# Optimization experiments

Measured on AMD Instinct MI355X. Metric: run time of the kernel, lower is better.

The kernel has to match this reference:

```python
import jax, jax.numpy as jnp
import numpy as np

N_NODES = 50000
N_EDGES = 800000
IN_DIM_N = 128
IN_DIM_E = 32
OUT_DIM = 128


def setup_inputs() -> dict:
    key = jax.random.key(0)
    k = jax.random.split(key, 6)
    nfeats = jax.random.normal(k[0], (N_NODES, IN_DIM_N), dtype=jnp.float32)
    efeats = jax.random.normal(k[1], (N_EDGES, IN_DIM_E), dtype=jnp.float32)
    # xavier-normal-ish scaling
    W_fc = jax.random.normal(k[2], (OUT_DIM, IN_DIM_N), dtype=jnp.float32) * (2.0 / np.sqrt(IN_DIM_N + OUT_DIM))
    W_attn = jax.random.normal(k[3], (1, 2 * OUT_DIM + IN_DIM_E), dtype=jnp.float32) * 0.08
    src = jax.random.randint(k[4], (N_EDGES,), 0, N_NODES, dtype=jnp.int32)
    dst = jax.random.randint(k[5], (N_EDGES,), 0, N_NODES, dtype=jnp.int32)
    return {"nfeats": nfeats, "efeats": efeats, "W_fc": W_fc, "W_attn": W_attn, "src": src, "dst": dst}


def reference(nfeats, efeats, W_fc, W_attn, src, dst):
    n_nodes = nfeats.shape[0]
    out_dim = W_fc.shape[0]
    in_dim_e = efeats.shape[1]

    # z = fc(nfeats)  [N, out_dim]
    z = nfeats @ W_fc.T

    # attn_fc(cat([z_src, efeats, z_dst])) split into three small dots
    a = W_attn[0]
    a_src = a[:out_dim]
    a_e = a[out_dim:out_dim + in_dim_e]
    a_dst = a[out_dim + in_dim_e:]
    s_src = z @ a_src            # [N]
    s_dst = z @ a_dst            # [N]
    s_e = efeats @ a_e           # [E]

    # per-edge attention logit + leaky_relu (torch default slope 0.01)
    e = jax.nn.leaky_relu(s_src[src] + s_e + s_dst[dst], negative_slope=0.01)  # [E]

    # segment softmax over incoming edges of each dst node
    m = jax.ops.segment_max(e, dst, num_segments=n_nodes)
    m = jnp.where(jnp.isfinite(m), m, 0.0)  # guard zero-degree nodes
    w = jnp.exp(e - m[dst])
    denom = jax.ops.segment_sum(w, dst, num_segments=n_nodes)
    alpha = w / jnp.where(denom > 0, denom, 1.0)[dst]  # [E]

    # weighted sum of source z into dst nodes
    h = jax.ops.segment_sum(alpha[:, None] * z[src], dst, num_segments=n_nodes)  # [N, out_dim]
    return h
```

## Files before the change

kernel.cpp:

```cpp
#include <hip/hip_runtime.h>
#include <math.h>

#define N_NODES 50000
#define N_EDGES 800000
#define IN_DIM_N 128
#define IN_DIM_E 32
#define OUT_DIM 128
#define SCAN_BLOCKS ((N_NODES + 255) / 256)
#define GEMM_BLOCKS ((N_NODES + 63) / 64)

typedef __bf16 bf16x8 __attribute__((ext_vector_type(8)));
typedef float  f32x4  __attribute__((ext_vector_type(4)));

__device__ inline unsigned bf16_rne(float x) {
    unsigned u = __float_as_uint(x);
    return (u + 0x7FFFu + ((u >> 16) & 1u)) >> 16;
}
__device__ inline unsigned pack_bf2(float a, float b) {
    return bf16_rne(a) | (bf16_rne(b) << 16);
}

__launch_bounds__(256)
__global__ void gemm_mfma_kernel(const float* __restrict__ A, const float* __restrict__ W,
                                 const float* __restrict__ attn,
                                 const int* __restrict__ dst, int* __restrict__ counts,
                                 unsigned* __restrict__ zb,
                                 float* __restrict__ s_src, float* __restrict__ s_dst) {
    __shared__ unsigned Au[64 * 68];
    __shared__ unsigned Bu[8192];
    __shared__ float asrc[128], adst[128];
    int tid = threadIdx.x;
    int row0 = blockIdx.x * 64;

    for (int i = tid; i < 2048; i += 256) {
        int fl = i & 63, tile = (i >> 6) & 7, ks = i >> 9;
        int n  = tile * 16 + (fl & 15);
        int kb = ks * 32 + (fl >> 4) * 8;
        const float* srcp = W + n * 128 + kb;
        unsigned o[4];
#pragma unroll
        for (int j = 0; j < 4; ++j) o[j] = pack_bf2(srcp[2 * j], srcp[2 * j + 1]);
        ((uint4*)Bu)[i] = *(uint4*)o;
    }
    if (tid < 128) { asrc[tid] = attn[tid]; adst[tid] = attn[160 + tid]; }

    for (int i = tid; i < 64 * 32; i += 256) {
        int r = i >> 5, q = i & 31;
        int gr = row0 + r;
        float4 v = make_float4(0.f, 0.f, 0.f, 0.f);
        if (gr < N_NODES) v = ((const float4*)A)[(long)gr * 32 + q];
        uint2 p = make_uint2(pack_bf2(v.x, v.y), pack_bf2(v.z, v.w));
        *((uint2*)&Au[r * 68 + q * 2]) = p;
    }
    __syncthreads();

    int lane = tid & 63;
    int wave = tid >> 6;
    int m = lane & 15, quad = lane >> 4;

    f32x4 acc[8];
#pragma unroll
    for (int t = 0; t < 8; ++t) acc[t] = (f32x4){0.f, 0.f, 0.f, 0.f};

#pragma unroll
    for (int ks = 0; ks < 4; ++ks) {
        uint4 au = *((const uint4*)&Au[(wave * 16 + m) * 68 + ks * 16 + quad * 4]);
        bf16x8 af = *(bf16x8*)&au;
#pragma unroll
        for (int t = 0; t < 8; ++t) {
            uint4 bu = *((const uint4*)&Bu[((ks * 8 + t) * 64 + lane) * 4]);
            bf16x8 bf = *(bf16x8*)&bu;
            acc[t] = __builtin_amdgcn_mfma_f32_16x16x32_bf16(af, bf, acc[t], 0, 0, 0);
        }
    }

    float ps[4] = {0.f, 0.f, 0.f, 0.f}, pd[4] = {0.f, 0.f, 0.f, 0.f};
#pragma unroll
    for (int t = 0; t < 8; ++t) {
        float as_ = asrc[t * 16 + m], ad_ = adst[t * 16 + m];
#pragma unroll
        for (int r = 0; r < 4; ++r) {
            float v = acc[t][r];
            ps[r] = fmaf(v, as_, ps[r]);
            pd[r] = fmaf(v, ad_, pd[r]);
            float vn = __shfl_xor(v, 1, 64);
            if (!(m & 1)) {
                int grow = row0 + wave * 16 + quad * 4 + r;
                if (grow < N_NODES)
                    zb[(long)grow * 64 + t * 8 + (m >> 1)] = pack_bf2(v, vn);
            }
        }
    }
#pragma unroll
    for (int r = 0; r < 4; ++r) {
        for (int off = 1; off < 16; off <<= 1) {
            ps[r] += __shfl_xor(ps[r], off, 64);
            pd[r] += __shfl_xor(pd[r], off, 64);
        }
    }
    if (m == 0) {
#pragma unroll
        for (int r = 0; r < 4; ++r) {
            int grow = row0 + wave * 16 + quad * 4 + r;
            if (grow < N_NODES) { s_src[grow] = ps[r]; s_dst[grow] = pd[r]; }
        }
    }

    for (int e = blockIdx.x * 256 + tid; e < N_EDGES; e += GEMM_BLOCKS * 256)
        atomicAdd(&counts[dst[e]], 1);
}

__launch_bounds__(256)
__global__ void scan1_kernel(const int* __restrict__ counts, int* __restrict__ offsets,
                             int* __restrict__ blocksums) {
    int i = blockIdx.x * 256 + threadIdx.x;
    int v = (i < N_NODES) ? counts[i] : 0;
    int lane = threadIdx.x & 63;
    int wv = threadIdx.x >> 6;
    int x = v;
    for (int off = 1; off < 64; off <<= 1) {
        int y = __shfl_up(x, off, 64);
        if (lane >= off) x += y;
    }
    __shared__ int wsum[4];
    if (lane == 63) wsum[wv] = x;
    __syncthreads();
    int base = 0;
    for (int w = 0; w < wv; ++w) base += wsum[w];
    if (i < N_NODES) offsets[i] = base + x - v;
    if (threadIdx.x == 255) blocksums[blockIdx.x] = base + x;
}

__launch_bounds__(256)
__global__ void scan2_kernel(int* __restrict__ blocksums) {
    int t = threadIdx.x;
    int v = (t < SCAN_BLOCKS) ? blocksums[t] : 0;
    int lane = t & 63;
    int wv = t >> 6;
    int x = v;
    for (int off = 1; off < 64; off <<= 1) {
        int y = __shfl_up(x, off, 64);
        if (lane >= off) x += y;
    }
    __shared__ int wsum[4];
    if (lane == 63) wsum[wv] = x;
    __syncthreads();
    int base = 0;
    for (int w = 0; w < wv; ++w) base += wsum[w];
    if (t < SCAN_BLOCKS) blocksums[t] = base + x - v;
}

__launch_bounds__(256)
__global__ void scan3_kernel(int* __restrict__ offsets, const int* __restrict__ blocksums,
                             int* __restrict__ cursor) {
    int i = blockIdx.x * 256 + threadIdx.x;
    if (i < N_NODES) {
        int v = offsets[i] + blocksums[blockIdx.x];
        offsets[i] = v;
        cursor[i] = v;
    }
    if (i == 0) offsets[N_NODES] = N_EDGES;
}

__global__ void score_scatter_kernel(const float* __restrict__ efeats, const float* __restrict__ attn,
                                     const int* __restrict__ src, const int* __restrict__ dst,
                                     const float* __restrict__ s_src, const float* __restrict__ s_dst,
                                     int* __restrict__ cursor, unsigned* __restrict__ pairs4) {
    int i = blockIdx.x * blockDim.x + threadIdx.x;
    if (i >= N_EDGES) return;
    const float4* ef = (const float4*)(efeats + (long)i * IN_DIM_E);
    const float4* ae = (const float4*)(attn + OUT_DIM);
    float se = 0.f;
#pragma unroll
    for (int q = 0; q < IN_DIM_E / 4; ++q) {
        float4 v = ef[q];
        float4 a = ae[q];
        se += v.x * a.x + v.y * a.y + v.z * a.z + v.w * a.w;
    }
    int s = src[i], d = dst[i];
    float x = s_src[s] + se + s_dst[d];
    float ev = (x >= 0.f) ? x : 0.01f * x;
    float w = expf(ev);
    int pos = atomicAdd(&cursor[d], 1);
    pairs4[pos] = (unsigned)s | (bf16_rne(w) << 16);
}

__launch_bounds__(256)
__global__ void aggregate_kernel(const unsigned* __restrict__ pairs4, const int* __restrict__ offsets,
                                 const unsigned* __restrict__ zb, float* __restrict__ h) {
    int node = blockIdx.x * 4 + (threadIdx.x >> 6);
    if (node >= N_NODES) return;
    int lane = threadIdx.x & 63;
    int beg = offsets[node], end = offsets[node + 1];
    float ax0 = 0.f, ay0 = 0.f, ax1 = 0.f, ay1 = 0.f;
    float ax2 = 0.f, ay2 = 0.f, ax3 = 0.f, ay3 = 0.f;
    float dsum = 0.f;
    for (int base = beg; base < end; base += 64) {
        int n = min(64, end - base);
        unsigned u = 0;
        if (lane < n) {
            u = pairs4[base + lane];
            dsum += __uint_as_float(u & 0xFFFF0000u);
        }
        int j = 0;
        for (; j + 3 < n; j += 4) {
            unsigned u0 = (unsigned)__shfl((int)u, j, 64);
            unsigned u1 = (unsigned)__shfl((int)u, j + 1, 64);
            unsigned u2 = (unsigned)__shfl((int)u, j + 2, 64);
            unsigned u3 = (unsigned)__shfl((int)u, j + 3, 64);
            unsigned z0 = zb[(long)(u0 & 0xFFFFu) * 64 + lane];
            unsigned z1 = zb[(long)(u1 & 0xFFFFu) * 64 + lane];
            unsigned z2 = zb[(long)(u2 & 0xFFFFu) * 64 + lane];
            unsigned z3 = zb[(long)(u3 & 0xFFFFu) * 64 + lane];
            float w0 = __uint_as_float(u0 & 0xFFFF0000u);
            float w1 = __uint_as_float(u1 & 0xFFFF0000u);
            float w2 = __uint_as_float(u2 & 0xFFFF0000u);
            float w3 = __uint_as_float(u3 & 0xFFFF0000u);
            ax0 = fmaf(w0, __uint_as_float(z0 << 16), ax0);
            ay0 = fmaf(w0, __uint_as_float(z0 & 0xFFFF0000u), ay0);
            ax1 = fmaf(w1, __uint_as_float(z1 << 16), ax1);
            ay1 = fmaf(w1, __uint_as_float(z1 & 0xFFFF0000u), ay1);
            ax2 = fmaf(w2, __uint_as_float(z2 << 16), ax2);
            ay2 = fmaf(w2, __uint_as_float(z2 & 0xFFFF0000u), ay2);
            ax3 = fmaf(w3, __uint_as_float(z3 << 16), ax3);
            ay3 = fmaf(w3, __uint_as_float(z3 & 0xFFFF0000u), ay3);
        }
        for (; j < n; ++j) {
            unsigned u0 = (unsigned)__shfl((int)u, j, 64);
            unsigned z0 = zb[(long)(u0 & 0xFFFFu) * 64 + lane];
            float w0 = __uint_as_float(u0 & 0xFFFF0000u);
            ax0 = fmaf(w0, __uint_as_float(z0 << 16), ax0);
            ay0 = fmaf(w0, __uint_as_float(z0 & 0xFFFF0000u), ay0);
        }
    }
    float accx = (ax0 + ax1) + (ax2 + ax3);
    float accy = (ay0 + ay1) + (ay2 + ay3);
    for (int off = 32; off; off >>= 1) dsum += __shfl_xor(dsum, off, 64);
    float scale = 1.f / (dsum > 0.f ? dsum : 1.f);
    ((float2*)h)[(long)node * 64 + lane] = make_float2(accx * scale, accy * scale);
}

extern "C" void kernel_launch(void* const* d_in, const int* in_sizes, int n_in,
                              void* d_out, int out_size, void* d_ws, size_t ws_size,
                              hipStream_t stream) {
    const float* nfeats = (const float*)d_in[0];
    const float* efeats = (const float*)d_in[1];
    const float* W_fc   = (const float*)d_in[2];
    const float* W_attn = (const float*)d_in[3];
    const int*   src    = (const int*)d_in[4];
    const int*   dst    = (const int*)d_in[5];
    float* h = (float*)d_out;

    char* ws = (char*)d_ws;
    unsigned* zb     = (unsigned*)ws;
    float* s_src     = (float*)(ws + (size_t)N_NODES * 64 * 4);
    float* s_dst     = s_src + N_NODES;
    int*   counts    = (int*)(s_dst + N_NODES);
    int*   offsets   = counts + N_NODES;
    int*   cursor    = offsets + N_NODES + 1;
    int*   blocksums = cursor + N_NODES;
    unsigned* pairs4 = (unsigned*)(blocksums + SCAN_BLOCKS + 4);

    hipMemsetAsync(counts, 0, N_NODES * sizeof(int), stream);
    gemm_mfma_kernel<<<GEMM_BLOCKS, 256, 0, stream>>>(
        nfeats, W_fc, W_attn, dst, counts, zb, s_src, s_dst);
    scan1_kernel<<<SCAN_BLOCKS, 256, 0, stream>>>(counts, offsets, blocksums);
    scan2_kernel<<<1, 256, 0, stream>>>(blocksums);
    scan3_kernel<<<SCAN_BLOCKS, 256, 0, stream>>>(offsets, blocksums, cursor);
    score_scatter_kernel<<<(N_EDGES + 255) / 256, 256, 0, stream>>>(
        efeats, W_attn, src, dst, s_src, s_dst, cursor, pairs4);
    aggregate_kernel<<<(N_NODES + 3) / 4, 256, 0, stream>>>(pairs4, offsets, zb, h);
}
```

Baseline: 302.8 us.

## Fuse histogram with edge scoring, record ranks, single-block scan, deterministic scatter

The dst histogram moves out of the GEMM kernel and into the edge-scoring kernel, where each edge's atomicAdd return value is saved as its rank along with a bf16 weight. The three-kernel scan becomes one 1024-thread block, and a separate scatter kernel then places each edge at offsets[d] + rank. The counts memset is folded into the GEMM kernel. This removes a second pass of atomics on the cursor and several launches, but adds reading and writing the rank and weight arrays, and the single-block scan does serial per-thread loops.

Measured after the change: 338.7 us. 11.9% more time.

```diff
diff --git a/kernel.cpp b/kernel.cpp
--- a/kernel.cpp
+++ b/kernel.cpp
@@ -6,7 +6,6 @@
 #define IN_DIM_N 128
 #define IN_DIM_E 32
 #define OUT_DIM 128
-#define SCAN_BLOCKS ((N_NODES + 255) / 256)
 #define GEMM_BLOCKS ((N_NODES + 63) / 64)
 
 typedef __bf16 bf16x8 __attribute__((ext_vector_type(8)));
@@ -23,14 +22,16 @@
 __launch_bounds__(256)
 __global__ void gemm_mfma_kernel(const float* __restrict__ A, const float* __restrict__ W,
                                  const float* __restrict__ attn,
-                                 const int* __restrict__ dst, int* __restrict__ counts,
-                                 unsigned* __restrict__ zb,
+                                 int* __restrict__ counts, unsigned* __restrict__ zb,
                                  float* __restrict__ s_src, float* __restrict__ s_dst) {
     __shared__ unsigned Au[64 * 68];
     __shared__ unsigned Bu[8192];
     __shared__ float asrc[128], adst[128];
     int tid = threadIdx.x;
     int row0 = blockIdx.x * 64;
+
+    int gid = blockIdx.x * 256 + tid;
+    if (gid < N_NODES) counts[gid] = 0;
 
     for (int i = tid; i < 2048; i += 256) {
         int fl = i & 63, tile = (i >> 6) & 7, ks = i >> 9;
@@ -105,67 +106,13 @@
             if (grow < N_NODES) { s_src[grow] = ps[r]; s_dst[grow] = pd[r]; }
         }
     }
-
-    for (int e = blockIdx.x * 256 + tid; e < N_EDGES; e += GEMM_BLOCKS * 256)
-        atomicAdd(&counts[dst[e]], 1);
-}
-
-__launch_bounds__(256)
-__global__ void scan1_kernel(const int* __restrict__ counts, int* __restrict__ offsets,
-                             int* __restrict__ blocksums) {
-    int i = blockIdx.x * 256 + threadIdx.x;
-    int v = (i < N_NODES) ? counts[i] : 0;
-    int lane = threadIdx.x & 63;
-    int wv = threadIdx.x >> 6;
-    int x = v;
-    for (int off = 1; off < 64; off <<= 1) {
-        int y = __shfl_up(x, off, 64);
-        if (lane >= off) x += y;
-    }
-    __shared__ int wsum[4];
-    if (lane == 63) wsum[wv] = x;
-    __syncthreads();
-    int base = 0;
-    for (int w = 0; w < wv; ++w) base += wsum[w];
-    if (i < N_NODES) offsets[i] = base + x - v;
-    if (threadIdx.x == 255) blocksums[blockIdx.x] = base + x;
-}
-
-__launch_bounds__(256)
-__global__ void scan2_kernel(int* __restrict__ blocksums) {
-    int t = threadIdx.x;
-    int v = (t < SCAN_BLOCKS) ? blocksums[t] : 0;
-    int lane = t & 63;
-    int wv = t >> 6;
-    int x = v;
-    for (int off = 1; off < 64; off <<= 1) {
-        int y = __shfl_up(x, off, 64);
-        if (lane >= off) x += y;
-    }
-    __shared__ int wsum[4];
-    if (lane == 63) wsum[wv] = x;
-    __syncthreads();
-    int base = 0;
-    for (int w = 0; w < wv; ++w) base += wsum[w];
-    if (t < SCAN_BLOCKS) blocksums[t] = base + x - v;
-}
-
-__launch_bounds__(256)
-__global__ void scan3_kernel(int* __restrict__ offsets, const int* __restrict__ blocksums,
-                             int* __restrict__ cursor) {
-    int i = blockIdx.x * 256 + threadIdx.x;
-    if (i < N_NODES) {
-        int v = offsets[i] + blocksums[blockIdx.x];
-        offsets[i] = v;
-        cursor[i] = v;
-    }
-    if (i == 0) offsets[N_NODES] = N_EDGES;
-}
-
-__global__ void score_scatter_kernel(const float* __restrict__ efeats, const float* __restrict__ attn,
-                                     const int* __restrict__ src, const int* __restrict__ dst,
-                                     const float* __restrict__ s_src, const float* __restrict__ s_dst,
-                                     int* __restrict__ cursor, unsigned* __restrict__ pairs4) {
+}
+
+__global__ void edge_score_hist_kernel(const float* __restrict__ efeats, const float* __restrict__ attn,
+                                       const int* __restrict__ src, const int* __restrict__ dst,
+                                       const float* __restrict__ s_src, const float* __restrict__ s_dst,
+                                       int* __restrict__ counts, unsigned short* __restrict__ ranks,
+                                       unsigned short* __restrict__ wq) {
     int i = blockIdx.x * blockDim.x + threadIdx.x;
     if (i >= N_EDGES) return;
     const float4* ef = (const float4*)(efeats + (long)i * IN_DIM_E);
@@ -181,8 +128,54 @@
     float x = s_src[s] + se + s_dst[d];
     float ev = (x >= 0.f) ? x : 0.01f * x;
     float w = expf(ev);
-    int pos = atomicAdd(&cursor[d], 1);
-    pairs4[pos] = (unsigned)s | (bf16_rne(w) << 16);
+    wq[i] = (unsigned short)bf16_rne(w);
+    ranks[i] = (unsigned short)atomicAdd(&counts[d], 1);
+}
+
+__launch_bounds__(1024)
+__global__ void scan_kernel(const int* __restrict__ counts, int* __restrict__ offsets) {
+    const int CHUNK = (N_NODES + 1023) / 1024;
+    int t = threadIdx.x;
+    int beg = t * CHUNK;
+    int end = min(beg + CHUNK, N_NODES);
+    int s = 0;
+    for (int i = beg; i < end; ++i) s += counts[i];
+
+    int lane = t & 63, wv = t >> 6;
+    int x = s;
+    for (int off = 1; off < 64; off <<= 1) {
+        int y = __shfl_up(x, off, 64);
+        if (lane >= off) x += y;
+    }
+    __shared__ int wsum[16], wbase[16];
+    if (lane == 63) wsum[wv] = x;
+    __syncthreads();
+    if (t < 16) {
+        int v = wsum[t];
+        for (int off = 1; off < 16; off <<= 1) {
+            int y = __shfl_up(v, off, 64);
+            if (t >= off) v += y;
+        }
+        wbase[t] = v - wsum[t];
+    }
+    __syncthreads();
+    int base = wbase[wv] + x - s;
+    for (int i = beg; i < end; ++i) {
+        offsets[i] = base;
+        base += counts[i];
+    }
+    if (t == 0) offsets[N_NODES] = N_EDGES;
+}
+
+__global__ void scatter_kernel(const int* __restrict__ src, const int* __restrict__ dst,
+                               const unsigned short* __restrict__ ranks,
+                               const unsigned short* __restrict__ wq,
+                               const int* __restrict__ offsets, unsigned* __restrict__ pairs4) {
+    int i = blockIdx.x * blockDim.x + threadIdx.x;
+    if (i >= N_EDGES) return;
+    int d = dst[i];
+    int pos = offsets[d] + (int)ranks[i];
+    pairs4[pos] = (unsigned)src[i] | ((unsigned)wq[i] << 16);
 }
 
 __launch_bounds__(256)
@@ -257,17 +250,16 @@
     float* s_dst     = s_src + N_NODES;
     int*   counts    = (int*)(s_dst + N_NODES);
     int*   offsets   = counts + N_NODES;
-    int*   cursor    = offsets + N_NODES + 1;
-    int*   blocksums = cursor + N_NODES;
-    unsigned* pairs4 = (unsigned*)(blocksums + SCAN_BLOCKS + 4);
-
-    hipMemsetAsync(counts, 0, N_NODES * sizeof(int), stream);
+    unsigned short* ranks = (unsigned short*)(offsets + N_NODES + 4);
+    unsigned short* wq    = ranks + N_EDGES;
+    unsigned* pairs4      = (unsigned*)(wq + N_EDGES);
+
     gemm_mfma_kernel<<<GEMM_BLOCKS, 256, 0, stream>>>(
-        nfeats, W_fc, W_attn, dst, counts, zb, s_src, s_dst);
-    scan1_kernel<<<SCAN_BLOCKS, 256, 0, stream>>>(counts, offsets, blocksums);
-    scan2_kernel<<<1, 256, 0, stream>>>(blocksums);
-    scan3_kernel<<<SCAN_BLOCKS, 256, 0, stream>>>(offsets, blocksums, cursor);
-    score_scatter_kernel<<<(N_EDGES + 255) / 256, 256, 0, stream>>>(
-        efeats, W_attn, src, dst, s_src, s_dst, cursor, pairs4);
+        nfeats, W_fc, W_attn, counts, zb, s_src, s_dst);
+    edge_score_hist_kernel<<<(N_EDGES + 255) / 256, 256, 0, stream>>>(
+        efeats, W_attn, src, dst, s_src, s_dst, counts, ranks, wq);
+    scan_kernel<<<1, 1024, 0, stream>>>(counts, offsets);
+    scatter_kernel<<<(N_EDGES + 255) / 256, 256, 0, stream>>>(
+        src, dst, ranks, wq, offsets, pairs4);
     aggregate_kernel<<<(N_NODES + 3) / 4, 256, 0, stream>>>(pairs4, offsets, zb, h);
 }
```

## Record per-edge rank during histogram to replace cursor atomics in scatter

Applied to the files above, without the earlier changes.

Moves the dst histogram out of the GEMM kernel into a new edge-scoring kernel that also records each edge's atomic rank and its bf16 weight. The scatter kernel then computes positions as offsets[dst] + rank with no atomics, and the counts memset is folded into the GEMM kernel. This removes one full pass of contended atomics over the edges and the cursor array. In exchange it adds 16-bit rank and weight buffers that are written and read back, and ranks are truncated to 16 bits, so a node with more than 65535 incoming edges would be placed wrongly. Folding the zeroing into the GEMM kernel also relies on every node index being covered by GEMM_BLOCKS*256 threads.

Result: faster. 270.3 us (-10.8%).

```diff
diff --git a/kernel.cpp b/kernel.cpp
--- a/kernel.cpp
+++ b/kernel.cpp
@@ -23,14 +23,16 @@
 __launch_bounds__(256)
 __global__ void gemm_mfma_kernel(const float* __restrict__ A, const float* __restrict__ W,
                                  const float* __restrict__ attn,
-                                 const int* __restrict__ dst, int* __restrict__ counts,
-                                 unsigned* __restrict__ zb,
+                                 int* __restrict__ counts, unsigned* __restrict__ zb,
                                  float* __restrict__ s_src, float* __restrict__ s_dst) {
     __shared__ unsigned Au[64 * 68];
     __shared__ unsigned Bu[8192];
     __shared__ float asrc[128], adst[128];
     int tid = threadIdx.x;
     int row0 = blockIdx.x * 64;
+
+    int gid = blockIdx.x * 256 + tid;
+    if (gid < N_NODES) counts[gid] = 0;
 
     for (int i = tid; i < 2048; i += 256) {
         int fl = i & 63, tile = (i >> 6) & 7, ks = i >> 9;
@@ -105,9 +107,30 @@
             if (grow < N_NODES) { s_src[grow] = ps[r]; s_dst[grow] = pd[r]; }
         }
     }
-
-    for (int e = blockIdx.x * 256 + tid; e < N_EDGES; e += GEMM_BLOCKS * 256)
-        atomicAdd(&counts[dst[e]], 1);
+}
+
+__global__ void edge_score_hist_kernel(const float* __restrict__ efeats, const float* __restrict__ attn,
+                                       const int* __restrict__ src, const int* __restrict__ dst,
+                                       const float* __restrict__ s_src, const float* __restrict__ s_dst,
+                                       int* __restrict__ counts, unsigned short* __restrict__ ranks,
+                                       unsigned short* __restrict__ wq) {
+    int i = blockIdx.x * blockDim.x + threadIdx.x;
+    if (i >= N_EDGES) return;
+    const float4* ef = (const float4*)(efeats + (long)i * IN_DIM_E);
+    const float4* ae = (const float4*)(attn + OUT_DIM);
+    float se = 0.f;
+#pragma unroll
+    for (int q = 0; q < IN_DIM_E / 4; ++q) {
+        float4 v = ef[q];
+        float4 a = ae[q];
+        se += v.x * a.x + v.y * a.y + v.z * a.z + v.w * a.w;
+    }
+    int s = src[i], d = dst[i];
+    float x = s_src[s] + se + s_dst[d];
+    float ev = (x >= 0.f) ? x : 0.01f * x;
+    float w = expf(ev);
+    wq[i] = (unsigned short)bf16_rne(w);
+    ranks[i] = (unsigned short)atomicAdd(&counts[d], 1);
 }
 
 __launch_bounds__(256)
@@ -151,38 +174,21 @@
 }
 
 __launch_bounds__(256)
-__global__ void scan3_kernel(int* __restrict__ offsets, const int* __restrict__ blocksums,
-                             int* __restrict__ cursor) {
+__global__ void scan3_kernel(int* __restrict__ offsets, const int* __restrict__ blocksums) {
     int i = blockIdx.x * 256 + threadIdx.x;
-    if (i < N_NODES) {
-        int v = offsets[i] + blocksums[blockIdx.x];
-        offsets[i] = v;
-        cursor[i] = v;
-    }
+    if (i < N_NODES) offsets[i] += blocksums[blockIdx.x];
     if (i == 0) offsets[N_NODES] = N_EDGES;
 }
 
-__global__ void score_scatter_kernel(const float* __restrict__ efeats, const float* __restrict__ attn,
-                                     const int* __restrict__ src, const int* __restrict__ dst,
-                                     const float* __restrict__ s_src, const float* __restrict__ s_dst,
-                                     int* __restrict__ cursor, unsigned* __restrict__ pairs4) {
+__global__ void scatter_kernel(const int* __restrict__ src, const int* __restrict__ dst,
+                               const unsigned short* __restrict__ ranks,
+                               const unsigned short* __restrict__ wq,
+                               const int* __restrict__ offsets, unsigned* __restrict__ pairs4) {
     int i = blockIdx.x * blockDim.x + threadIdx.x;
     if (i >= N_EDGES) return;
-    const float4* ef = (const float4*)(efeats + (long)i * IN_DIM_E);
-    const float4* ae = (const float4*)(attn + OUT_DIM);
-    float se = 0.f;
-#pragma unroll
-    for (int q = 0; q < IN_DIM_E / 4; ++q) {
-        float4 v = ef[q];
-        float4 a = ae[q];
-        se += v.x * a.x + v.y * a.y + v.z * a.z + v.w * a.w;
-    }
-    int s = src[i], d = dst[i];
-    float x = s_src[s] + se + s_dst[d];
-    float ev = (x >= 0.f) ? x : 0.01f * x;
-    float w = expf(ev);
-    int pos = atomicAdd(&cursor[d], 1);
-    pairs4[pos] = (unsigned)s | (bf16_rne(w) << 16);
+    int d = dst[i];
+    int pos = offsets[d] + (int)ranks[i];
+    pairs4[pos] = (unsigned)src[i] | ((unsigned)wq[i] << 16);
 }
 
 __launch_bounds__(256)
@@ -257,17 +263,19 @@
     float* s_dst     = s_src + N_NODES;
     int*   counts    = (int*)(s_dst + N_NODES);
     int*   offsets   = counts + N_NODES;
-    int*   cursor    = offsets + N_NODES + 1;
-    int*   blocksums = cursor + N_NODES;
-    unsigned* pairs4 = (unsigned*)(blocksums + SCAN_BLOCKS + 4);
-
-    hipMemsetAsync(counts, 0, N_NODES * sizeof(int), stream);
+    int*   blocksums = offsets + N_NODES + 1;
+    unsigned short* ranks = (unsigned short*)(blocksums + SCAN_BLOCKS + 4);
+    unsigned short* wq    = ranks + N_EDGES;
+    unsigned* pairs4      = (unsigned*)(wq + N_EDGES);
+
     gemm_mfma_kernel<<<GEMM_BLOCKS, 256, 0, stream>>>(
-        nfeats, W_fc, W_attn, dst, counts, zb, s_src, s_dst);
+        nfeats, W_fc, W_attn, counts, zb, s_src, s_dst);
+    edge_score_hist_kernel<<<(N_EDGES + 255) / 256, 256, 0, stream>>>(
+        efeats, W_attn, src, dst, s_src, s_dst, counts, ranks, wq);
     scan1_kernel<<<SCAN_BLOCKS, 256, 0, stream>>>(counts, offsets, blocksums);
     scan2_kernel<<<1, 256, 0, stream>>>(blocksums);
-    scan3_kernel<<<SCAN_BLOCKS, 256, 0, stream>>>(offsets, blocksums, cursor);
-    score_scatter_kernel<<<(N_EDGES + 255) / 256, 256, 0, stream>>>(
-        efeats, W_attn, src, dst, s_src, s_dst, cursor, pairs4);
+    scan3_kernel<<<SCAN_BLOCKS, 256, 0, stream>>>(offsets, blocksums);
+    scatter_kernel<<<(N_EDGES + 255) / 256, 256, 0, stream>>>(
+        src, dst, ranks, wq, offsets, pairs4);
     aggregate_kernel<<<(N_NODES + 3) / 4, 256, 0, stream>>>(pairs4, offsets, zb, h);
 }
```

## Precompute bf16 W fragments, split histogram kernel, fold scan3 into consumers

Applied to the files above, without the earlier changes.

A small kernel now converts W_fc to bf16 MFMA fragments once and zeroes the counts array, replacing the memset. The GEMM reads B fragments from global memory instead of rebuilding a 32KB LDS copy in every block, which should raise occupancy and remove redundant conversion work. The dst histogram moves to its own kernel. The scan3 pass is removed: scan1 writes block-local offsets and cursors, and score_scatter and aggregate add blocksums on the fly. The cost is extra global/L2 traffic for B fragments and one more index lookup per edge and per node.

Measured after the change: 309.1 us. +2.1%, slower.

```diff
diff --git a/kernel.cpp b/kernel.cpp
--- a/kernel.cpp
+++ b/kernel.cpp
@@ -20,28 +20,37 @@
     return bf16_rne(a) | (bf16_rne(b) << 16);
 }
 
-__launch_bounds__(256)
-__global__ void gemm_mfma_kernel(const float* __restrict__ A, const float* __restrict__ W,
-                                 const float* __restrict__ attn,
-                                 const int* __restrict__ dst, int* __restrict__ counts,
-                                 unsigned* __restrict__ zb,
+__global__ void wfrag_kernel(const float* __restrict__ W, unsigned* __restrict__ Wfrag,
+                             int* __restrict__ counts) {
+    int t = blockIdx.x * 256 + threadIdx.x;
+    for (int i = t; i < N_NODES; i += 2048) counts[i] = 0;
+    if (t >= 2048) return;
+    int lane = t & 63;
+    int tile = (t >> 6) & 7;
+    int ks   = t >> 9;
+    int n  = tile * 16 + (lane & 15);
+    int kb = ks * 32 + (lane >> 4) * 8;
+    const float* srcp = W + n * 128 + kb;
+    unsigned o[4];
+#pragma unroll
+    for (int j = 0; j < 4; ++j) o[j] = pack_bf2(srcp[2 * j], srcp[2 * j + 1]);
+    ((uint4*)Wfrag)[t] = *(uint4*)o;
+}
+
+__global__ void hist_kernel(const int* __restrict__ dst, int* __restrict__ counts) {
+    int i = blockIdx.x * blockDim.x + threadIdx.x;
+    if (i < N_EDGES) atomicAdd(&counts[dst[i]], 1);
+}
+
+__launch_bounds__(256)
+__global__ void gemm_mfma_kernel(const float* __restrict__ A, const unsigned* __restrict__ Wfrag,
+                                 const float* __restrict__ attn, unsigned* __restrict__ zb,
                                  float* __restrict__ s_src, float* __restrict__ s_dst) {
     __shared__ unsigned Au[64 * 68];
-    __shared__ unsigned Bu[8192];
     __shared__ float asrc[128], adst[128];
     int tid = threadIdx.x;
     int row0 = blockIdx.x * 64;
 
-    for (int i = tid; i < 2048; i += 256) {
-        int fl = i & 63, tile = (i >> 6) & 7, ks = i >> 9;
-        int n  = tile * 16 + (fl & 15);
-        int kb = ks * 32 + (fl >> 4) * 8;
-        const float* srcp = W + n * 128 + kb;
-        unsigned o[4];
-#pragma unroll
-        for (int j = 0; j < 4; ++j) o[j] = pack_bf2(srcp[2 * j], srcp[2 * j + 1]);
-        ((uint4*)Bu)[i] = *(uint4*)o;
-    }
     if (tid < 128) { asrc[tid] = attn[tid]; adst[tid] = attn[160 + tid]; }
 
     for (int i = tid; i < 64 * 32; i += 256) {
@@ -57,6 +66,7 @@
     int lane = tid & 63;
     int wave = tid >> 6;
     int m = lane & 15, quad = lane >> 4;
+    const uint4* Wg = (const uint4*)Wfrag;
 
     f32x4 acc[8];
 #pragma unroll
@@ -68,7 +78,7 @@
         bf16x8 af = *(bf16x8*)&au;
 #pragma unroll
         for (int t = 0; t < 8; ++t) {
-            uint4 bu = *((const uint4*)&Bu[((ks * 8 + t) * 64 + lane) * 4]);
+            uint4 bu = Wg[(ks * 8 + t) * 64 + lane];
             bf16x8 bf = *(bf16x8*)&bu;
             acc[t] = __builtin_amdgcn_mfma_f32_16x16x32_bf16(af, bf, acc[t], 0, 0, 0);
         }
@@ -105,14 +115,11 @@
             if (grow < N_NODES) { s_src[grow] = ps[r]; s_dst[grow] = pd[r]; }
         }
     }
-
-    for (int e = blockIdx.x * 256 + tid; e < N_EDGES; e += GEMM_BLOCKS * 256)
-        atomicAdd(&counts[dst[e]], 1);
 }
 
 __launch_bounds__(256)
 __global__ void scan1_kernel(const int* __restrict__ counts, int* __restrict__ offsets,
-                             int* __restrict__ blocksums) {
+                             int* __restrict__ cursor, int* __restrict__ blocksums) {
     int i = blockIdx.x * 256 + threadIdx.x;
     int v = (i < N_NODES) ? counts[i] : 0;
     int lane = threadIdx.x & 63;
@@ -127,7 +134,9 @@
     __syncthreads();
     int base = 0;
     for (int w = 0; w < wv; ++w) base += wsum[w];
-    if (i < N_NODES) offsets[i] = base + x - v;
+    int excl = base + x - v;
+    if (i <= N_NODES) offsets[i] = excl;
+    if (i < N_NODES) cursor[i] = excl;
     if (threadIdx.x == 255) blocksums[blockIdx.x] = base + x;
 }
 
@@ -150,22 +159,11 @@
     if (t < SCAN_BLOCKS) blocksums[t] = base + x - v;
 }
 
-__launch_bounds__(256)
-__global__ void scan3_kernel(int* __restrict__ offsets, const int* __restrict__ blocksums,
-                             int* __restrict__ cursor) {
-    int i = blockIdx.x * 256 + threadIdx.x;
-    if (i < N_NODES) {
-        int v = offsets[i] + blocksums[blockIdx.x];
-        offsets[i] = v;
-        cursor[i] = v;
-    }
-    if (i == 0) offsets[N_NODES] = N_EDGES;
-}
-
 __global__ void score_scatter_kernel(const float* __restrict__ efeats, const float* __restrict__ attn,
                                      const int* __restrict__ src, const int* __restrict__ dst,
                                      const float* __restrict__ s_src, const float* __restrict__ s_dst,
-                                     int* __restrict__ cursor, unsigned* __restrict__ pairs4) {
+                                     int* __restrict__ cursor, const int* __restrict__ blocksums,
+                                     unsigned* __restrict__ pairs4) {
     int i = blockIdx.x * blockDim.x + threadIdx.x;
     if (i >= N_EDGES) return;
     const float4* ef = (const float4*)(efeats + (long)i * IN_DIM_E);
@@ -181,17 +179,19 @@
     float x = s_src[s] + se + s_dst[d];
     float ev = (x >= 0.f) ? x : 0.01f * x;
     float w = expf(ev);
-    int pos = atomicAdd(&cursor[d], 1);
+    int pos = atomicAdd(&cursor[d], 1) + blocksums[d >> 8];
     pairs4[pos] = (unsigned)s | (bf16_rne(w) << 16);
 }
 
 __launch_bounds__(256)
 __global__ void aggregate_kernel(const unsigned* __restrict__ pairs4, const int* __restrict__ offsets,
+                                 const int* __restrict__ blocksums,
                                  const unsigned* __restrict__ zb, float* __restrict__ h) {
     int node = blockIdx.x * 4 + (threadIdx.x >> 6);
     if (node >= N_NODES) return;
     int lane = threadIdx.x & 63;
-    int beg = offsets[node], end = offsets[node + 1];
+    int beg = offsets[node] + blocksums[node >> 8];
+    int end = offsets[node + 1] + blocksums[(node + 1) >> 8];
     float ax0 = 0.f, ay0 = 0.f, ax1 = 0.f, ay1 = 0.f;
     float ax2 = 0.f, ay2 = 0.f, ax3 = 0.f, ay3 = 0.f;
     float dsum = 0.f;
@@ -255,19 +255,20 @@
     unsigned* zb     = (unsigned*)ws;
     float* s_src     = (float*)(ws + (size_t)N_NODES * 64 * 4);
     float* s_dst     = s_src + N_NODES;
-    int*   counts    = (int*)(s_dst + N_NODES);
+    unsigned* Wfrag  = (unsigned*)(s_dst + N_NODES);
+    int*   counts    = (int*)(Wfrag + 8192);
     int*   offsets   = counts + N_NODES;
-    int*   cursor    = offsets + N_NODES + 1;
+    int*   cursor    = offsets + N_NODES + 4;
     int*   blocksums = cursor + N_NODES;
     unsigned* pairs4 = (unsigned*)(blocksums + SCAN_BLOCKS + 4);
 
-    hipMemsetAsync(counts, 0, N_NODES * sizeof(int), stream);
+    wfrag_kernel<<<8, 256, 0, stream>>>(W_fc, Wfrag, counts);
+    hist_kernel<<<(N_EDGES + 255) / 256, 256, 0, stream>>>(dst, counts);
     gemm_mfma_kernel<<<GEMM_BLOCKS, 256, 0, stream>>>(
-        nfeats, W_fc, W_attn, dst, counts, zb, s_src, s_dst);
-    scan1_kernel<<<SCAN_BLOCKS, 256, 0, stream>>>(counts, offsets, blocksums);
+        nfeats, Wfrag, W_attn, zb, s_src, s_dst);
+    scan1_kernel<<<SCAN_BLOCKS, 256, 0, stream>>>(counts, offsets, cursor, blocksums);
     scan2_kernel<<<1, 256, 0, stream>>>(blocksums);
-    scan3_kernel<<<SCAN_BLOCKS, 256, 0, stream>>>(offsets, blocksums, cursor);
     score_scatter_kernel<<<(N_EDGES + 255) / 256, 256, 0, stream>>>(
-        efeats, W_attn, src, dst, s_src, s_dst, cursor, pairs4);
-    aggregate_kernel<<<(N_NODES + 3) / 4, 256, 0, stream>>>(pairs4, offsets, zb, h);
-}
+        efeats, W_attn, src, dst, s_src, s_dst, cursor, blocksums, pairs4);
+    aggregate_kernel<<<(N_NODES + 3) / 4, 256, 0, stream>>>(pairs4, offsets, blocksums, zb, h);
+}
```
